# Optimization experiments

Measured on AMD Instinct MI355X. Metric: run time of the kernel, lower is better.

Reference implementation:

```python
import jax, jax.numpy as jnp
import numpy as np

N_NODES = 100_000
N_EDGES = 1_600_000
F_NODE = 4
F_EDGE = 5
H = 64
EDGE_DIM = 2 * H + F_EDGE  # 133


def setup_inputs() -> dict:
    key = jax.random.key(0)
    ks = jax.random.split(key, 24)
    s = 0.05
    inp = {
        "node_feat": jax.random.normal(ks[0], (N_NODES, F_NODE), jnp.float32),
        "edge_feat": jax.random.normal(ks[1], (N_EDGES, F_EDGE), jnp.float32),
        "src": jax.random.randint(ks[2], (N_EDGES,), 0, N_NODES, jnp.int32),
        "dst": jax.random.randint(ks[3], (N_EDGES,), 0, N_NODES, jnp.int32),
        # SAGEConv 1 (DGL mean aggregator: fc_self(h) + fc_neigh(mean_neigh(h)) + bias)
        "W1s": jax.random.normal(ks[4], (F_NODE, H), jnp.float32) * s,
        "W1n": jax.random.normal(ks[5], (F_NODE, H), jnp.float32) * s,
        "b1": jnp.zeros((H,), jnp.float32),
        # SAGEConv 2
        "W2s": jax.random.normal(ks[6], (H, H), jnp.float32) * s,
        "W2n": jax.random.normal(ks[7], (H, H), jnp.float32) * s,
        "b2": jnp.zeros((H,), jnp.float32),
        # nodeprocess: Linear(F_NODE? no -> applied to h which is H-dim) Linear(H? )
        # NOTE: original declares nn.Linear(num_node_features, hidden) but applies it to h (H-dim);
        # we follow the applied shape, Linear(H, H), so the math is runnable and consistent.
        "Wnp": jax.random.normal(ks[8], (H, H), jnp.float32) * s,
        "bnp": jnp.zeros((H,), jnp.float32),
        # edgeprocess: Linear(EDGE_DIM, H) -> tanh -> Linear(H, 1)
        "We1": jax.random.normal(ks[9], (EDGE_DIM, H), jnp.float32) * s,
        "be1": jnp.zeros((H,), jnp.float32),
        "We2": jax.random.normal(ks[10], (H, 1), jnp.float32) * s,
        "be2": jnp.zeros((1,), jnp.float32),
        # lin1: Linear(EDGE_DIM, H); lin2: Linear(H, 1)
        "Wl1": jax.random.normal(ks[11], (EDGE_DIM, H), jnp.float32) * s,
        "bl1": jnp.zeros((H,), jnp.float32),
        "Wl2": jax.random.normal(ks[12], (H, 1), jnp.float32) * s,
        "bl2": jnp.zeros((1,), jnp.float32),
    }
    return inp


def _sage_mean(h, src, dst, Ws, Wn, b, inv_deg):
    # project first (cheaper: N x d instead of E x d), then gather+scatter-mean
    msg = (h @ Wn)[src]                                    # [E, H]
    agg = jax.ops.segment_sum(msg, dst, num_segments=h.shape[0]) * inv_deg
    return h @ Ws + agg + b


def reference(node_feat, edge_feat, src, dst,
              W1s, W1n, b1, W2s, W2n, b2,
              Wnp, bnp, We1, be1, We2, be2,
              Wl1, bl1, Wl2, bl2):
    n = node_feat.shape[0]
    deg = jax.ops.segment_sum(jnp.ones_like(dst, jnp.float32), dst, num_segments=n)
    inv_deg = (1.0 / jnp.maximum(deg, 1.0))[:, None]       # [N,1]

    h = jax.nn.relu(_sage_mean(node_feat, src, dst, W1s, W1n, b1, inv_deg))
    h = jax.nn.relu(_sage_mean(h, src, dst, W2s, W2n, b2, inv_deg))

    h_src = jax.nn.relu(h[src] @ Wnp + bnp)                # [E, H]
    h_dst = jax.nn.relu(h[dst] @ Wnp + bnp)                # [E, H]
    ef = jnp.concatenate([h_src, h_dst, edge_feat], axis=1)  # [E, 133]

    w = jax.nn.sigmoid(jnp.tanh(ef @ We1 + be1) @ We2 + be2)  # [E, 1]
    efw = ef * w
    out = jax.nn.relu(efw @ Wl1 + bl1)                     # dropout: eval mode (identity)
    return out @ Wl2 + bl2                                 # [E, 1]
```

## Files before the change

kernel.cpp:

```cpp
#include <hip/hip_runtime.h>
#include <math.h>


__device__ __forceinline__ float fast_tanh(float x) {
    x = fminf(fmaxf(x, -15.f), 15.f);
    float e2 = __expf(2.f * x);
    return (e2 - 1.f) * __builtin_amdgcn_rcpf(e2 + 1.f);
}
__device__ __forceinline__ float fast_sigmoid(float x) {
    x = fminf(fmaxf(x, -60.f), 60.f);
    return __builtin_amdgcn_rcpf(1.f + __expf(-x));
}
__device__ __forceinline__ unsigned short f2bf(float f) {
    unsigned u = __float_as_uint(f);
    u = u + 0x7FFFu + ((u >> 16) & 1u);
    return (unsigned short)(u >> 16);
}
__device__ __forceinline__ unsigned pack2bf(float lo, float hi) {
    return ((unsigned)f2bf(hi) << 16) | (unsigned)f2bf(lo);
}
__device__ __forceinline__ float bflo(unsigned u) { return __uint_as_float(u << 16); }
__device__ __forceinline__ float bfhi(unsigned u) { return __uint_as_float(u & 0xFFFF0000u); }

__device__ __forceinline__ float dpp_sum16(float x) {
    int t;
    t = __builtin_amdgcn_update_dpp(0, __float_as_int(x), 0xB1, 0xF, 0xF, true);
    x += __int_as_float(t);
    t = __builtin_amdgcn_update_dpp(0, __float_as_int(x), 0x4E, 0xF, 0xF, true);
    x += __int_as_float(t);
    t = __builtin_amdgcn_update_dpp(0, __float_as_int(x), 0x141, 0xF, 0xF, true);
    x += __int_as_float(t);
    t = __builtin_amdgcn_update_dpp(0, __float_as_int(x), 0x140, 0xF, 0xF, true);
    x += __int_as_float(t);
    return x;
}

__global__ void rank_k(const int* __restrict__ dst, int* __restrict__ deg,
                       int* __restrict__ rank, int E) {
    int e = blockIdx.x * blockDim.x + threadIdx.x;
    if (e < E) rank[e] = atomicAdd(&deg[dst[e]], 1);
}

__global__ void scan1_k(const int* __restrict__ deg, int* __restrict__ off,
                        int* __restrict__ bsum, int N) {
    __shared__ int tmp[256];
    int i = blockIdx.x * 256 + threadIdx.x;
    int v = (i < N) ? deg[i] : 0;
    tmp[threadIdx.x] = v;
    __syncthreads();
#pragma unroll
    for (int s = 1; s < 256; s <<= 1) {
        int t = (threadIdx.x >= s) ? tmp[threadIdx.x - s] : 0;
        __syncthreads();
        tmp[threadIdx.x] += t;
        __syncthreads();
    }
    if (i < N) off[i] = tmp[threadIdx.x] - v;
    if (threadIdx.x == 255) bsum[blockIdx.x] = tmp[255];
}

__global__ void scan2_k(int* __restrict__ bsum, int nb) {
    __shared__ int tmp[512];
    int i = threadIdx.x;
    int v = (i < nb) ? bsum[i] : 0;
    tmp[i] = v;
    __syncthreads();
#pragma unroll
    for (int s = 1; s < 512; s <<= 1) {
        int t = (i >= s) ? tmp[i - s] : 0;
        __syncthreads();
        tmp[i] += t;
        __syncthreads();
    }
    if (i < nb) bsum[i] = tmp[i] - v;
}

__global__ void scan3_k(int* __restrict__ off, const int* __restrict__ bsum,
                        int N, int E) {
    int i = blockIdx.x * 256 + threadIdx.x;
    if (i < N) off[i] += bsum[blockIdx.x];
    if (i == 0) off[N] = E;
}

__global__ void fill2_k(const int* __restrict__ src, const int* __restrict__ dst,
                        const int* __restrict__ off, const int* __restrict__ rank,
                        int2* __restrict__ csr, int E) {
    int e = blockIdx.x * blockDim.x + threadIdx.x;
    if (e >= E) return;
    csr[off[dst[e]] + rank[e]] = make_int2(src[e], e);
}

__global__ __launch_bounds__(256, 8)
void aggh1f_k(const int* __restrict__ off, const int2* __restrict__ csr,
              const float* __restrict__ nf,
              const float* __restrict__ W1s, const float* __restrict__ W1n,
              const float* __restrict__ b1, unsigned short* __restrict__ h1s, int N) {
    int n = blockIdx.x * 4 + (threadIdx.x >> 6);
    if (n >= N) return;
    int l = threadIdx.x & 63;
    int s0 = off[n], s1 = off[n + 1];
    float4 a = {0.f, 0.f, 0.f, 0.f};
    for (int i = s0 + l; i < s1; i += 64) {
        float4 r = ((const float4*)nf)[csr[i].x];
        a.x += r.x; a.y += r.y; a.z += r.z; a.w += r.w;
    }
#pragma unroll
    for (int m = 1; m < 64; m <<= 1) {
        a.x += __shfl_xor(a.x, m);
        a.y += __shfl_xor(a.y, m);
        a.z += __shfl_xor(a.z, m);
        a.w += __shfl_xor(a.w, m);
    }
    float invd = 1.f / fmaxf((float)(s1 - s0), 1.f);
    a.x *= invd; a.y *= invd; a.z *= invd; a.w *= invd;
    float4 r = ((const float4*)nf)[n];
    float v = b1[l]
            + r.x * W1s[l] + r.y * W1s[64 + l] + r.z * W1s[128 + l] + r.w * W1s[192 + l]
            + a.x * W1n[l] + a.y * W1n[64 + l] + a.z * W1n[128 + l] + a.w * W1n[192 + l];
    h1s[(size_t)n * 64 + l] = f2bf(fmaxf(v, 0.f));
}

__global__ __launch_bounds__(256, 8)
void gatherh1_k(const int* __restrict__ off, const int2* __restrict__ csr,
                const uint4* __restrict__ h1b4, uint4* __restrict__ ah1b4, int N) {
    int n = blockIdx.x * 4 + (threadIdx.x >> 6);
    if (n >= N) return;
    int l = threadIdx.x & 63;
    int g = l >> 3, q = l & 7;
    int s0 = off[n], s1 = off[n + 1];
    float a0 = 0.f, a1 = 0.f, a2 = 0.f, a3 = 0.f;
    float a4 = 0.f, a5 = 0.f, a6 = 0.f, a7 = 0.f;
    int i = s0;
    for (; i + 8 <= s1; i += 8) {
        int r = csr[i + g].x;
        uint4 v = h1b4[(size_t)r * 8 + q];
        a0 += bflo(v.x); a1 += bfhi(v.x);
        a2 += bflo(v.y); a3 += bfhi(v.y);
        a4 += bflo(v.z); a5 += bfhi(v.z);
        a6 += bflo(v.w); a7 += bfhi(v.w);
    }
    int rem = s1 - i;
    if (g < rem) {
        int r = csr[i + g].x;
        uint4 v = h1b4[(size_t)r * 8 + q];
        a0 += bflo(v.x); a1 += bfhi(v.x);
        a2 += bflo(v.y); a3 += bfhi(v.y);
        a4 += bflo(v.z); a5 += bfhi(v.z);
        a6 += bflo(v.w); a7 += bfhi(v.w);
    }
#pragma unroll
    for (int m = 8; m <= 32; m <<= 1) {
        a0 += __shfl_xor(a0, m); a1 += __shfl_xor(a1, m);
        a2 += __shfl_xor(a2, m); a3 += __shfl_xor(a3, m);
        a4 += __shfl_xor(a4, m); a5 += __shfl_xor(a5, m);
        a6 += __shfl_xor(a6, m); a7 += __shfl_xor(a7, m);
    }
    if (l < 8) {
        float invd = 1.f / fmaxf((float)(s1 - s0), 1.f);
        uint4 pk;
        pk.x = pack2bf(a0 * invd, a1 * invd);
        pk.y = pack2bf(a2 * invd, a3 * invd);
        pk.z = pack2bf(a4 * invd, a5 * invd);
        pk.w = pack2bf(a6 * invd, a7 * invd);
        ah1b4[(size_t)n * 8 + q] = pk;
    }
}

__device__ __forceinline__ void mac64(const float (*hT)[68], const float (*wt)[64],
                                      int rr, int cr, float acc[4][4]) {
#pragma unroll 8
    for (int k = 0; k < 64; ++k) {
        float4 a = *(const float4*)&hT[k][rr];
        float4 w = *(const float4*)&wt[k][cr];
        acc[0][0] = fmaf(a.x, w.x, acc[0][0]); acc[0][1] = fmaf(a.x, w.y, acc[0][1]);
        acc[0][2] = fmaf(a.x, w.z, acc[0][2]); acc[0][3] = fmaf(a.x, w.w, acc[0][3]);
        acc[1][0] = fmaf(a.y, w.x, acc[1][0]); acc[1][1] = fmaf(a.y, w.y, acc[1][1]);
        acc[1][2] = fmaf(a.y, w.z, acc[1][2]); acc[1][3] = fmaf(a.y, w.w, acc[1][3]);
        acc[2][0] = fmaf(a.z, w.x, acc[2][0]); acc[2][1] = fmaf(a.z, w.y, acc[2][1]);
        acc[2][2] = fmaf(a.z, w.z, acc[2][2]); acc[2][3] = fmaf(a.z, w.w, acc[2][3]);
        acc[3][0] = fmaf(a.w, w.x, acc[3][0]); acc[3][1] = fmaf(a.w, w.y, acc[3][1]);
        acc[3][2] = fmaf(a.w, w.z, acc[3][2]); acc[3][3] = fmaf(a.w, w.w, acc[3][3]);
    }
}

__global__ __launch_bounds__(256, 4)
void node_mlp_k(const unsigned* __restrict__ h1b, const unsigned* __restrict__ ah1b,
                const float* __restrict__ W2s, const float* __restrict__ W2n,
                const float* __restrict__ b2, const float* __restrict__ Wnp,
                const float* __restrict__ bnp, const float* __restrict__ We1,
                const float* __restrict__ Wl1, unsigned short* __restrict__ ST, int N) {
    __shared__ __align__(16) float hT[64][68];
    __shared__ __align__(16) float wt[64][64];
    const int t = threadIdx.x;
    const int m0 = blockIdx.x * 64;
    const int cr = (t & 15) << 2, rr = (t >> 4) << 2;
    float acc[4][4] = {};

#pragma unroll
    for (int it = 0; it < 8; ++it) {
        int u = it * 256 + t;
        int m = u >> 5, p = u & 31;
        int row = m0 + m;
        unsigned v = (row < N) ? h1b[(size_t)row * 32 + p] : 0u;
        hT[2 * p][m] = bflo(v);
        hT[2 * p + 1][m] = bfhi(v);
    }
#pragma unroll
    for (int it = 0; it < 16; ++it) {
        int k = it * 4 + (t >> 6), c = t & 63;
        wt[k][c] = W2s[k * 64 + c];
    }
    __syncthreads();
    mac64(hT, wt, rr, cr, acc);
    __syncthreads();

#pragma unroll
    for (int it = 0; it < 8; ++it) {
        int u = it * 256 + t;
        int m = u >> 5, p = u & 31;
        int row = m0 + m;
        unsigned v = (row < N) ? ah1b[(size_t)row * 32 + p] : 0u;
        hT[2 * p][m] = bflo(v);
        hT[2 * p + 1][m] = bfhi(v);
    }
#pragma unroll
    for (int it = 0; it < 16; ++it) {
        int k = it * 4 + (t >> 6), c = t & 63;
        wt[k][c] = W2n[k * 64 + c];
    }
    __syncthreads();
    mac64(hT, wt, rr, cr, acc);
    __syncthreads();

#pragma unroll
    for (int i = 0; i < 4; ++i)
#pragma unroll
        for (int q = 0; q < 4; ++q)
            hT[cr + q][rr + i] = fmaxf(acc[i][q] + b2[cr + q], 0.f);
#pragma unroll
    for (int it = 0; it < 16; ++it) {
        int k = it * 4 + (t >> 6), c = t & 63;
        wt[k][c] = Wnp[k * 64 + c];
    }
    __syncthreads();
    float ac2[4][4] = {};
    mac64(hT, wt, rr, cr, ac2);
    __syncthreads();

#pragma unroll
    for (int i = 0; i < 4; ++i)
#pragma unroll
        for (int q = 0; q < 4; ++q)
            hT[cr + q][rr + i] = fmaxf(ac2[i][q] + bnp[cr + q], 0.f);
    __syncthreads();

    for (int cb = 0; cb < 4; ++cb) {
        if (cb) __syncthreads();
#pragma unroll
        for (int it = 0; it < 16; ++it) {
            int k = it * 4 + (t >> 6), c = t & 63;
            int cglob = cb * 64 + c;
            int half = cglob >> 7, cc = cglob & 127;
            int jj = cc >> 1, p = cc & 1;
            const float* W = p ? Wl1 : We1;
            wt[k][c] = W[(half * 64 + k) * 64 + jj];
        }
        __syncthreads();
        float ac3[4][4] = {};
        mac64(hT, wt, rr, cr, ac3);
#pragma unroll
        for (int i = 0; i < 4; ++i) {
            int row = m0 + rr + i;
            if (row >= N) continue;
            ushort4 pk;
            pk.x = f2bf(ac3[i][0]); pk.y = f2bf(ac3[i][1]);
            pk.z = f2bf(ac3[i][2]); pk.w = f2bf(ac3[i][3]);
            *(ushort4*)&ST[(size_t)row * 256 + cb * 64 + cr] = pk;
        }
    }
}

__global__ void edge_k(const int* __restrict__ off, const int2* __restrict__ csr,
                       const float* __restrict__ ef, const unsigned* __restrict__ ST32,
                       const float* __restrict__ We1, const float* __restrict__ be1,
                       const float* __restrict__ We2, const float* __restrict__ be2,
                       const float* __restrict__ Wl1, const float* __restrict__ bl1,
                       const float* __restrict__ Wl2, const float* __restrict__ bl2,
                       float* __restrict__ out, int N) {
    int n = blockIdx.x * 4 + (threadIdx.x >> 6);
    if (n >= N) return;
    const int l = threadIdx.x & 63;
    const int g = l >> 4;
    const int q = l & 15;
    const int j0 = q << 2;
    int s0 = off[n], s1 = off[n + 1];
    if (s0 >= s1) return;

    float4 wet[5], wlt[5];
#pragma unroll
    for (int k = 0; k < 5; ++k) {
        wet[k] = *(const float4*)&We1[(128 + k) * 64 + j0];
        wlt[k] = *(const float4*)&Wl1[(128 + k) * 64 + j0];
    }
    const float4 vbe1 = *(const float4*)&be1[j0];
    const float4 vwe2 = *(const float4*)&We2[j0];
    const float4 vbl1 = *(const float4*)&bl1[j0];
    const float4 vwl2 = *(const float4*)&Wl2[j0];
    const float vbe2 = be2[0], vbl2 = bl2[0];

    uint4 pw = *(const uint4*)&ST32[(size_t)n * 128 + 64 + j0];
    const float4 tb = {bflo(pw.x) + vbe1.x, bflo(pw.y) + vbe1.y,
                       bflo(pw.z) + vbe1.z, bflo(pw.w) + vbe1.w};
    const float4 ub = {bfhi(pw.x), bfhi(pw.y), bfhi(pw.z), bfhi(pw.w)};

    const bool gb1 = (g & 1), gb2 = (g & 2);

    for (int i = s0; i < s1; i += 4) {
        int ii = i + g;
        bool act = ii < s1;
        int2 se = csr[act ? ii : s0];
        uint4 sw = *(const uint4*)&ST32[(size_t)se.x * 128 + j0];
        float4 t4 = {bflo(sw.x) + tb.x, bflo(sw.y) + tb.y,
                     bflo(sw.z) + tb.z, bflo(sw.w) + tb.w};
        float4 u4 = {bfhi(sw.x) + ub.x, bfhi(sw.y) + ub.y,
                     bfhi(sw.z) + ub.z, bfhi(sw.w) + ub.w};
        int e0 = __builtin_amdgcn_readlane(se.y, 0);
        int e1 = __builtin_amdgcn_readlane(se.y, 16);
        int e2 = __builtin_amdgcn_readlane(se.y, 32);
        int e3 = __builtin_amdgcn_readlane(se.y, 48);
        const float* p0 = ef + (size_t)e0 * 5;
        const float* p1 = ef + (size_t)e1 * 5;
        const float* p2 = ef + (size_t)e2 * 5;
        const float* p3 = ef + (size_t)e3 * 5;
#pragma unroll
        for (int k = 0; k < 5; ++k) {
            float a01 = gb1 ? p1[k] : p0[k];
            float a23 = gb1 ? p3[k] : p2[k];
            float ek  = gb2 ? a23 : a01;
            t4.x = fmaf(ek, wet[k].x, t4.x); t4.y = fmaf(ek, wet[k].y, t4.y);
            t4.z = fmaf(ek, wet[k].z, t4.z); t4.w = fmaf(ek, wet[k].w, t4.w);
            u4.x = fmaf(ek, wlt[k].x, u4.x); u4.y = fmaf(ek, wlt[k].y, u4.y);
            u4.z = fmaf(ek, wlt[k].z, u4.z); u4.w = fmaf(ek, wlt[k].w, u4.w);
        }
        float z = fast_tanh(t4.x) * vwe2.x + fast_tanh(t4.y) * vwe2.y
                + fast_tanh(t4.z) * vwe2.z + fast_tanh(t4.w) * vwe2.w;
        z = dpp_sum16(z);
        float w = fast_sigmoid(z + vbe2);
        float o = fmaxf(fmaf(w, u4.x, vbl1.x), 0.f) * vwl2.x
                + fmaxf(fmaf(w, u4.y, vbl1.y), 0.f) * vwl2.y
                + fmaxf(fmaf(w, u4.z, vbl1.z), 0.f) * vwl2.z
                + fmaxf(fmaf(w, u4.w, vbl1.w), 0.f) * vwl2.w;
        o = dpp_sum16(o);
        if (q == 0 && act) out[se.y] = o + vbl2;
    }
}

extern "C" void kernel_launch(void* const* d_in, const int* in_sizes, int n_in,
                              void* d_out, int out_size, void* d_ws, size_t ws_size,
                              hipStream_t stream) {
    const float* nf  = (const float*)d_in[0];
    const float* ef  = (const float*)d_in[1];
    const int*   src = (const int*)d_in[2];
    const int*   dst = (const int*)d_in[3];
    const float* W1s = (const float*)d_in[4];
    const float* W1n = (const float*)d_in[5];
    const float* b1  = (const float*)d_in[6];
    const float* W2s = (const float*)d_in[7];
    const float* W2n = (const float*)d_in[8];
    const float* b2  = (const float*)d_in[9];
    const float* Wnp = (const float*)d_in[10];
    const float* bnp = (const float*)d_in[11];
    const float* We1 = (const float*)d_in[12];
    const float* be1 = (const float*)d_in[13];
    const float* We2 = (const float*)d_in[14];
    const float* be2 = (const float*)d_in[15];
    const float* Wl1 = (const float*)d_in[16];
    const float* bl1 = (const float*)d_in[17];
    const float* Wl2 = (const float*)d_in[18];
    const float* bl2 = (const float*)d_in[19];

    const int N = in_sizes[0] / 4;
    const int E = in_sizes[2];

    float* wsf = (float*)d_ws;
    unsigned short* ST = (unsigned short*)wsf;
    unsigned* ah1b = (unsigned*)(wsf + (size_t)128 * N);
    unsigned* h1b  = (unsigned*)(wsf + (size_t)192 * N);
    int2* csr  = (int2*)(wsf + (size_t)224 * N);
    int*  rank = (int*)(wsf + (size_t)256 * N);
    int*  deg  = (int*)(wsf + (size_t)272 * N);
    int*  off  = deg + N;
    int*  bsum = off + N + 1;
    float* out = (float*)d_out;

    const int nblkN1 = (N + 255) / 256;
    const int nblkE  = (E + 255) / 256;
    const int nblkNw4 = (N + 3) / 4;
    const int gemmx  = (N + 63) / 64;

    hipMemsetAsync(deg, 0, (size_t)N * sizeof(int), stream);
    rank_k<<<nblkE, 256, 0, stream>>>(dst, deg, rank, E);
    scan1_k<<<nblkN1, 256, 0, stream>>>(deg, off, bsum, N);
    scan2_k<<<1, 512, 0, stream>>>(bsum, nblkN1);
    scan3_k<<<nblkN1, 256, 0, stream>>>(off, bsum, N, E);
    fill2_k<<<nblkE, 256, 0, stream>>>(src, dst, off, rank, csr, E);

    aggh1f_k<<<nblkNw4, 256, 0, stream>>>(off, csr, nf, W1s, W1n, b1,
                                          (unsigned short*)h1b, N);

    gatherh1_k<<<nblkNw4, 256, 0, stream>>>(off, csr, (const uint4*)h1b,
                                            (uint4*)ah1b, N);

    node_mlp_k<<<gemmx, 256, 0, stream>>>(h1b, ah1b, W2s, W2n, b2,
                                          Wnp, bnp, We1, Wl1, ST, N);

    edge_k<<<nblkNw4, 256, 0, stream>>>(off, csr, ef, (const unsigned*)ST,
                                        We1, be1, We2, be2, Wl1, bl1, Wl2, bl2,
                                        out, N);
}
```

Before: 543.9 us.

## Switch edge kernel to grid-stride edge chunks and unroll neighbor gather

The edge kernel no longer assigns one wave per destination node. It now uses a fixed grid of 2048 blocks that stride over 4-edge chunks of the CSR array, which is meant to remove load imbalance and the idle lanes left at the tail of each node's edge list. In exchange, each edge must look up its destination through the dst array and load that node's precomputed row, where the old code loaded it once per node. The neighbor gather in gatherh1 also gains a 16-wide unrolled loop so two row loads are in flight per iteration.

```diff
diff --git a/kernel.cpp b/kernel.cpp
--- a/kernel.cpp
+++ b/kernel.cpp
@@ -131,6 +131,16 @@
     float a0 = 0.f, a1 = 0.f, a2 = 0.f, a3 = 0.f;
     float a4 = 0.f, a5 = 0.f, a6 = 0.f, a7 = 0.f;
     int i = s0;
+    for (; i + 16 <= s1; i += 16) {
+        int r0 = csr[i + g].x;
+        int r1 = csr[i + 8 + g].x;
+        uint4 v0 = h1b4[(size_t)r0 * 8 + q];
+        uint4 v1 = h1b4[(size_t)r1 * 8 + q];
+        a0 += bflo(v0.x) + bflo(v1.x); a1 += bfhi(v0.x) + bfhi(v1.x);
+        a2 += bflo(v0.y) + bflo(v1.y); a3 += bfhi(v0.y) + bfhi(v1.y);
+        a4 += bflo(v0.z) + bflo(v1.z); a5 += bfhi(v0.z) + bfhi(v1.z);
+        a6 += bflo(v0.w) + bflo(v1.w); a7 += bfhi(v0.w) + bfhi(v1.w);
+    }
     for (; i + 8 <= s1; i += 8) {
         int r = csr[i + g].x;
         uint4 v = h1b4[(size_t)r * 8 + q];
@@ -280,21 +290,18 @@
     }
 }
 
-__global__ void edge_k(const int* __restrict__ off, const int2* __restrict__ csr,
+__global__ void edge_k(const int2* __restrict__ csr, const int* __restrict__ dstarr,
                        const float* __restrict__ ef, const unsigned* __restrict__ ST32,
                        const float* __restrict__ We1, const float* __restrict__ be1,
                        const float* __restrict__ We2, const float* __restrict__ be2,
                        const float* __restrict__ Wl1, const float* __restrict__ bl1,
                        const float* __restrict__ Wl2, const float* __restrict__ bl2,
-                       float* __restrict__ out, int N) {
-    int n = blockIdx.x * 4 + (threadIdx.x >> 6);
-    if (n >= N) return;
+                       float* __restrict__ out, int E, int nwaves) {
     const int l = threadIdx.x & 63;
     const int g = l >> 4;
     const int q = l & 15;
     const int j0 = q << 2;
-    int s0 = off[n], s1 = off[n + 1];
-    if (s0 >= s1) return;
+    const int wid = blockIdx.x * (blockDim.x >> 6) + (threadIdx.x >> 6);
 
     float4 wet[5], wlt[5];
 #pragma unroll
@@ -308,22 +315,22 @@
     const float4 vwl2 = *(const float4*)&Wl2[j0];
     const float vbe2 = be2[0], vbl2 = bl2[0];
 
-    uint4 pw = *(const uint4*)&ST32[(size_t)n * 128 + 64 + j0];
-    const float4 tb = {bflo(pw.x) + vbe1.x, bflo(pw.y) + vbe1.y,
-                       bflo(pw.z) + vbe1.z, bflo(pw.w) + vbe1.w};
-    const float4 ub = {bfhi(pw.x), bfhi(pw.y), bfhi(pw.z), bfhi(pw.w)};
-
     const bool gb1 = (g & 1), gb2 = (g & 2);
-
-    for (int i = s0; i < s1; i += 4) {
-        int ii = i + g;
-        bool act = ii < s1;
-        int2 se = csr[act ? ii : s0];
+    const int nch = (E + 3) >> 2;
+
+    for (int c = wid; c < nch; c += nwaves) {
+        int slot = c * 4 + g;
+        bool act = slot < E;
+        int2 se = csr[act ? slot : (E - 1)];
+        int dn = dstarr[se.y];
+        uint4 pw = *(const uint4*)&ST32[(size_t)dn * 128 + 64 + j0];
         uint4 sw = *(const uint4*)&ST32[(size_t)se.x * 128 + j0];
-        float4 t4 = {bflo(sw.x) + tb.x, bflo(sw.y) + tb.y,
-                     bflo(sw.z) + tb.z, bflo(sw.w) + tb.w};
-        float4 u4 = {bfhi(sw.x) + ub.x, bfhi(sw.y) + ub.y,
-                     bfhi(sw.z) + ub.z, bfhi(sw.w) + ub.w};
+        float4 t4 = {bflo(sw.x) + bflo(pw.x) + vbe1.x,
+                     bflo(sw.y) + bflo(pw.y) + vbe1.y,
+                     bflo(sw.z) + bflo(pw.z) + vbe1.z,
+                     bflo(sw.w) + bflo(pw.w) + vbe1.w};
+        float4 u4 = {bfhi(sw.x) + bfhi(pw.x), bfhi(sw.y) + bfhi(pw.y),
+                     bfhi(sw.z) + bfhi(pw.z), bfhi(sw.w) + bfhi(pw.w)};
         int e0 = __builtin_amdgcn_readlane(se.y, 0);
         int e1 = __builtin_amdgcn_readlane(se.y, 16);
         int e2 = __builtin_amdgcn_readlane(se.y, 32);
@@ -397,6 +404,8 @@
     const int nblkE  = (E + 255) / 256;
     const int nblkNw4 = (N + 3) / 4;
     const int gemmx  = (N + 63) / 64;
+    const int EDGE_BLOCKS = 2048;
+    const int nwaves = EDGE_BLOCKS * 4;
 
     hipMemsetAsync(deg, 0, (size_t)N * sizeof(int), stream);
     rank_k<<<nblkE, 256, 0, stream>>>(dst, deg, rank, E);
@@ -414,7 +423,7 @@
     node_mlp_k<<<gemmx, 256, 0, stream>>>(h1b, ah1b, W2s, W2n, b2,
                                           Wnp, bnp, We1, Wl1, ST, N);
 
-    edge_k<<<nblkNw4, 256, 0, stream>>>(off, csr, ef, (const unsigned*)ST,
-                                        We1, be1, We2, be2, Wl1, bl1, Wl2, bl2,
-                                        out, N);
-}
+    edge_k<<<EDGE_BLOCKS, 256, 0, stream>>>(csr, dst, ef, (const unsigned*)ST,
+                                            We1, be1, We2, be2, Wl1, bl1, Wl2, bl2,
+                                            out, E, nwaves);
+}
```

New measurement: 523.9 us. -3.7%, faster.
